# Kernel tuning notes

Hardware: AMD Instinct MI355X
Metric: run time of the kernel (lower is better)

The kernel has to match this reference:

```python
import jax, jax.numpy as jnp
import numpy as np

N_HEADS = 32
N_KV_HEADS = 8
HEAD_DIM = 128
DIM = 4096
ROPE_THETA = 500000.0
B, S = 2, 2048


def setup_inputs() -> dict:
    key = jax.random.key(0)
    k1, k2, k3, k4, k5 = jax.random.split(key, 5)
    sd = 0.02
    return {
        "x": jax.random.normal(k1, (B, S, DIM), dtype=jnp.float32),
        "wq": jax.random.normal(k2, (DIM, N_HEADS * HEAD_DIM), dtype=jnp.float32) * sd,
        "wk": jax.random.normal(k3, (DIM, N_KV_HEADS * HEAD_DIM), dtype=jnp.float32) * sd,
        "wv": jax.random.normal(k4, (DIM, N_KV_HEADS * HEAD_DIM), dtype=jnp.float32) * sd,
        "wo": jax.random.normal(k5, (N_HEADS * HEAD_DIM, DIM), dtype=jnp.float32) * sd,
    }


def _rope_freqs(seqlen, head_dim, theta):
    inv = 1.0 / (theta ** (jnp.arange(0, head_dim, 2, dtype=jnp.float32) / head_dim))
    ang = jnp.arange(seqlen, dtype=jnp.float32)[:, None] * inv[None, :]  # [S, hd/2]
    return jnp.cos(ang), jnp.sin(ang)


def _apply_rope(t, cos, sin):
    # t: [B, S, H, hd]; complex multiply on interleaved (even, odd) pairs
    tr = t.reshape(*t.shape[:-1], HEAD_DIM // 2, 2)
    a, b = tr[..., 0], tr[..., 1]
    c = cos[None, :, None, :]
    s = sin[None, :, None, :]
    out = jnp.stack([a * c - b * s, a * s + b * c], axis=-1)
    return out.reshape(t.shape)


def reference(x, wq, wk, wv, wo):
    bsz, seqlen, _ = x.shape
    n_rep = N_HEADS // N_KV_HEADS
    q = (x @ wq).reshape(bsz, seqlen, N_HEADS, HEAD_DIM)
    k = (x @ wk).reshape(bsz, seqlen, N_KV_HEADS, HEAD_DIM)
    v = (x @ wv).reshape(bsz, seqlen, N_KV_HEADS, HEAD_DIM)

    cos, sin = _rope_freqs(seqlen, HEAD_DIM, ROPE_THETA)
    q = _apply_rope(q, cos, sin)
    k = _apply_rope(k, cos, sin)

    # repeat_kv: expand kv heads to n_heads (torch.repeat_interleave dim=2)
    k = jnp.repeat(k, n_rep, axis=2)  # [B, S, H, hd]
    v = jnp.repeat(v, n_rep, axis=2)

    scale = 1.0 / jnp.sqrt(jnp.float32(HEAD_DIM))
    scores = jnp.einsum("bqhd,bkhd->bhqk", q, k) * scale  # [B, H, S, S]
    causal = jnp.tril(jnp.ones((seqlen, seqlen), dtype=bool))
    scores = jnp.where(causal[None, None], scores, jnp.float32(-1e9))
    probs = jax.nn.softmax(scores, axis=-1)
    out = jnp.einsum("bhqk,bkhd->bqhd", probs, v)  # [B, S, H, hd]
    out = out.reshape(bsz, seqlen, N_HEADS * HEAD_DIM)
    return out @ wo
```

## Files before the change

kernel.cpp:

```cpp
#include <hip/hip_runtime.h>
#include <stdint.h>

typedef unsigned short u16;
using short8 = __attribute__((ext_vector_type(8))) short;
using f32x4  = __attribute__((ext_vector_type(4))) float;

#define S_LEN 2048
#define NH 32
#define NKV 8
#define HD 128
#define DIM 4096
#define NQ 4096
#define NKVD 1024

typedef __attribute__((address_space(1))) unsigned int uGLB;
typedef __attribute__((address_space(3))) unsigned int uLDS;

__device__ __forceinline__ void g2l16(const u16* g, u16* l) {
  __builtin_amdgcn_global_load_lds((const uGLB*)g, (uLDS*)l, 16, 0, 0);
}

__device__ __forceinline__ float b2f(u16 u) {
  union { unsigned u32; float f; } x; x.u32 = ((unsigned)u) << 16; return x.f;
}
__device__ __forceinline__ u16 f2b(float f) {
  union { float f; unsigned u32; } x; x.f = f;
  unsigned lsb = (x.u32 >> 16) & 1u;
  x.u32 += 0x7fffu + lsb;
  return (u16)(x.u32 >> 16);
}

__global__ __launch_bounds__(256) void transpose_cast(const float* __restrict__ in,
                                                      u16* __restrict__ out,
                                                      int K, int N) {
  __shared__ float tile[32][33];
  int n0 = blockIdx.x * 32, k0 = blockIdx.y * 32;
  int tx = threadIdx.x, ty = threadIdx.y;
#pragma unroll
  for (int j = 0; j < 4; ++j)
    tile[ty + j * 8][tx] = in[(size_t)(k0 + ty + j * 8) * N + n0 + tx];
  __syncthreads();
#pragma unroll
  for (int j = 0; j < 4; ++j)
    out[(size_t)(n0 + ty + j * 8) * K + k0 + tx] = f2b(tile[tx][ty + j * 8]);
}

__global__ __launch_bounds__(256) void cast_x(const float* __restrict__ in,
                                              u16* __restrict__ out, int n4) {
  int i = blockIdx.x * 256 + threadIdx.x;
  if (i >= n4) return;
  float4 v = reinterpret_cast<const float4*>(in)[i];
  ushort4 u;
  u.x = f2b(v.x); u.y = f2b(v.y); u.z = f2b(v.z); u.w = f2b(v.w);
  reinterpret_cast<ushort4*>(out)[i] = u;
}

__global__ __launch_bounds__(256, 2) void gemm_bt(const u16* __restrict__ A,
                                                  const u16* __restrict__ Bt,
                                                  int N, int mode,
                                                  float* __restrict__ out,
                                                  u16* __restrict__ Qb,
                                                  u16* __restrict__ Kb,
                                                  u16* __restrict__ Vt) {
  const int K = 4096;
  __shared__ __align__(16) u16 As[128 * 32];
  __shared__ __align__(16) u16 Bs[128 * 32];
  int tid  = threadIdx.x;
  int m0   = blockIdx.y * 128, n0 = blockIdx.x * 128;
  int lane = tid & 63, w = tid >> 6;
  int wr   = w >> 1, wc = w & 1;
  int ml   = lane & 15, quad = lane >> 4;

  f32x4 acc[4][4] = {};

  for (int k0 = 0; k0 < K; k0 += 32) {
    __syncthreads();
#pragma unroll
    for (int p = 0; p < 2; ++p) {
      int slot = w * 128 + p * 64 + lane;
      int row = slot >> 2, ch = slot & 3;
      int src = ch ^ ((row >> 1) & 3);
      g2l16(A + (size_t)(m0 + row) * K + k0 + src * 8, &As[(w * 128 + p * 64) * 8]);
      g2l16(Bt + (size_t)(n0 + row) * K + k0 + src * 8, &Bs[(w * 128 + p * 64) * 8]);
    }
    __syncthreads();
    short8 af[4], bfr[4];
#pragma unroll
    for (int mi = 0; mi < 4; ++mi) {
      int row = wr * 64 + mi * 16 + ml;
      int ch = quad ^ ((row >> 1) & 3);
      af[mi] = *reinterpret_cast<const short8*>(&As[row * 32 + ch * 8]);
    }
#pragma unroll
    for (int ni = 0; ni < 4; ++ni) {
      int row = wc * 64 + ni * 16 + ml;
      int ch = quad ^ ((row >> 1) & 3);
      bfr[ni] = *reinterpret_cast<const short8*>(&Bs[row * 32 + ch * 8]);
    }
#pragma unroll
    for (int mi = 0; mi < 4; ++mi)
#pragma unroll
      for (int ni = 0; ni < 4; ++ni)
        acc[mi][ni] = __builtin_amdgcn_mfma_f32_16x16x32_bf16(af[mi], bfr[ni], acc[mi][ni], 0, 0, 0);
  }

#pragma unroll
  for (int mi = 0; mi < 4; ++mi) {
#pragma unroll
    for (int ni = 0; ni < 4; ++ni) {
#pragma unroll
      for (int r = 0; r < 4; ++r) {
        int row = m0 + wr * 64 + mi * 16 + quad * 4 + r;
        int col = n0 + wc * 64 + ni * 16 + ml;
        float v = acc[mi][ni][r];
        if (mode == 1) {
          out[(size_t)row * N + col] = v;
        } else {
          int b = row >> 11, s = row & (S_LEN - 1);
          if (col < NQ) {
            int h = col >> 7, d = col & 127;
            Qb[((size_t)((b * NH + h) * S_LEN + s)) * HD + d] = f2b(v);
          } else if (col < NQ + NKVD) {
            int cc = col - NQ; int h = cc >> 7, d = cc & 127;
            Kb[((size_t)((b * NKV + h) * S_LEN + s)) * HD + d] = f2b(v);
          } else {
            int cc = col - NQ - NKVD; int h = cc >> 7, d = cc & 127;
            Vt[((size_t)((b * NKV + h) * HD + d)) * S_LEN + s] = f2b(v);
          }
        }
      }
    }
  }
}

__global__ __launch_bounds__(256) void rope_ip(u16* __restrict__ X, int npairs) {
  int idx = blockIdx.x * 256 + threadIdx.x;
  if (idx >= npairs) return;
  int i = idx & 63;
  int s = (idx >> 6) & (S_LEN - 1);
  float inv = __expf(-0.2050369278939421f * (float)i);
  float ang = (float)s * inv;
  float sn, cs;
  sincosf(ang, &sn, &cs);
  ushort2 pr = reinterpret_cast<ushort2*>(X)[idx];
  float a = b2f(pr.x), b = b2f(pr.y);
  ushort2 o;
  o.x = f2b(a * cs - b * sn);
  o.y = f2b(a * sn + b * cs);
  reinterpret_cast<ushort2*>(X)[idx] = o;
}

__global__ __launch_bounds__(256, 3) void flash(const u16* __restrict__ Qb,
                                                const u16* __restrict__ Kb,
                                                const u16* __restrict__ Vt,
                                                u16* __restrict__ AO) {
  __shared__ __align__(16) u16 Ks[64 * 128];
  __shared__ __align__(16) u16 Vs[128 * 64];
  __shared__ __align__(16) u16 Ps[4 * 16 * 80];

  int tid  = threadIdx.x;
  int lane = tid & 63, w = tid >> 6;
  int ml   = lane & 15, quad = lane >> 4;
  int q_tile = blockIdx.x, h = blockIdx.y, b = blockIdx.z;
  int hkv = h >> 2;
  int q0  = q_tile * 64;
  const u16* Qh = Qb + ((size_t)(b * NH + h) * S_LEN) * HD;
  const u16* Kh = Kb + ((size_t)(b * NKV + hkv) * S_LEN) * HD;
  const u16* Vh = Vt + ((size_t)(b * NKV + hkv) * HD) * S_LEN;
  u16* Pw = Ps + w * 16 * 80;

  short8 qf[4];
#pragma unroll
  for (int ks = 0; ks < 4; ++ks)
    qf[ks] = *reinterpret_cast<const short8*>(
        Qh + (size_t)(q0 + w * 16 + ml) * HD + ks * 32 + quad * 8);

  short8 ones8;
  {
    u16 one_b = 0x3f80;
#pragma unroll
    for (int j = 0; j < 8; ++j) ones8[j] = (short)one_b;
  }

  f32x4 o[8] = {};
  f32x4 o9 = {};
  const float SC = 0.12751745f;
  const float BIAS = 18.0f;

  int qg = q0 + w * 16 + ml;
  int ntile = q_tile + 1;
  for (int it = 0; it < ntile; ++it) {
    int kv0 = it * 64;
    __syncthreads();
#pragma unroll
    for (int p = 0; p < 4; ++p) {
      int slot = w * 256 + p * 64 + lane;
      int krow = slot >> 4, kch = slot & 15;
      int ksrc = kch ^ (krow & 15);
      g2l16(Kh + (size_t)(kv0 + krow) * HD + ksrc * 8, &Ks[(w * 256 + p * 64) * 8]);
      int vrow = slot >> 3, vch = slot & 7;
      int vsrc = vch ^ (vrow & 7);
      g2l16(Vh + (size_t)vrow * S_LEN + kv0 + vsrc * 8, &Vs[(w * 256 + p * 64) * 8]);
    }
    __syncthreads();

    f32x4 st[4] = {};
#pragma unroll
    for (int ks = 0; ks < 4; ++ks) {
#pragma unroll
      for (int nt = 0; nt < 4; ++nt) {
        int row = nt * 16 + ml;
        int ch = ((ks << 2) | quad) ^ ml;
        short8 kf = *reinterpret_cast<const short8*>(&Ks[row * 128 + ch * 8]);
        st[nt] = __builtin_amdgcn_mfma_f32_16x16x32_bf16(kf, qf[ks], st[nt], 0, 0, 0);
      }
    }

    bool diag = (it == q_tile);
#pragma unroll
    for (int nt = 0; nt < 4; ++nt) {
      float p0 = exp2f(fmaf(st[nt][0], SC, -BIAS));
      float p1 = exp2f(fmaf(st[nt][1], SC, -BIAS));
      float p2 = exp2f(fmaf(st[nt][2], SC, -BIAS));
      float p3 = exp2f(fmaf(st[nt][3], SC, -BIAS));
      if (diag) {
        int kg = kv0 + nt * 16 + quad * 4;
        if (kg + 0 > qg) p0 = 0.f;
        if (kg + 1 > qg) p1 = 0.f;
        if (kg + 2 > qg) p2 = 0.f;
        if (kg + 3 > qg) p3 = 0.f;
      }
      uint2 pk;
      pk.x = (unsigned)f2b(p0) | ((unsigned)f2b(p1) << 16);
      pk.y = (unsigned)f2b(p2) | ((unsigned)f2b(p3) << 16);
      *reinterpret_cast<uint2*>(&Pw[ml * 80 + nt * 16 + quad * 4]) = pk;
    }

#pragma unroll
    for (int ks2 = 0; ks2 < 2; ++ks2) {
      short8 pf = *reinterpret_cast<const short8*>(&Pw[ml * 80 + ks2 * 32 + quad * 8]);
#pragma unroll
      for (int dt = 0; dt < 8; ++dt) {
        int row = dt * 16 + ml;
        int ch = ((ks2 << 2) | quad) ^ (ml & 7);
        short8 vf = *reinterpret_cast<const short8*>(&Vs[row * 64 + ch * 8]);
        o[dt] = __builtin_amdgcn_mfma_f32_16x16x32_bf16(pf, vf, o[dt], 0, 0, 0);
      }
      o9 = __builtin_amdgcn_mfma_f32_16x16x32_bf16(pf, ones8, o9, 0, 0, 0);
    }
  }

  size_t row_base = (size_t)(b * S_LEN + q0 + w * 16 + quad * 4);
#pragma unroll
  for (int r = 0; r < 4; ++r) {
    float inv_l = 1.0f / o9[r];
#pragma unroll
    for (int dt = 0; dt < 8; ++dt) {
      int col = h * HD + dt * 16 + ml;
      AO[(row_base + r) * (size_t)DIM + col] = f2b(o[dt][r] * inv_l);
    }
  }
}

extern "C" void kernel_launch(void* const* d_in, const int* in_sizes, int n_in,
                              void* d_out, int out_size, void* d_ws, size_t ws_size,
                              hipStream_t stream) {
  const float* x  = (const float*)d_in[0];
  const float* wq = (const float*)d_in[1];
  const float* wk = (const float*)d_in[2];
  const float* wv = (const float*)d_in[3];
  const float* wo = (const float*)d_in[4];
  float* out = (float*)d_out;
  char* ws = (char*)d_ws;

  u16* Wqt = (u16*)(ws + 0);
  u16* Wkt = (u16*)(ws + 33554432);
  u16* Wvt = (u16*)(ws + 41943040);
  u16* Xb  = (u16*)(ws + 50331648);
  u16* Qb  = (u16*)(ws + 83886080);
  u16* Kb  = (u16*)(ws + 117440512);
  u16* Vt  = (u16*)(ws + 125829120);

  transpose_cast<<<dim3(128, 128), dim3(32, 8), 0, stream>>>(wq, Wqt, 4096, 4096);
  transpose_cast<<<dim3(32, 128),  dim3(32, 8), 0, stream>>>(wk, Wkt, 4096, 1024);
  transpose_cast<<<dim3(32, 128),  dim3(32, 8), 0, stream>>>(wv, Wvt, 4096, 1024);
  cast_x<<<16384, 256, 0, stream>>>(x, Xb, 4194304);

  gemm_bt<<<dim3(48, 32), 256, 0, stream>>>(Xb, Wqt, 6144, 0, nullptr, Qb, Kb, Vt);

  rope_ip<<<32768, 256, 0, stream>>>(Qb, 8388608);
  rope_ip<<<8192, 256, 0, stream>>>(Kb, 2097152);

  transpose_cast<<<dim3(128, 128), dim3(32, 8), 0, stream>>>(wo, Wqt, 4096, 4096);

  flash<<<dim3(32, 32, 2), 256, 0, stream>>>(Qb, Kb, Vt, Xb);

  gemm_bt<<<dim3(32, 32), 256, 0, stream>>>(Xb, Wqt, 4096, 1, out, nullptr, nullptr, nullptr);
}
```

Measured before the change: 874.0 us.

## Replace 128x128 GEMM with 256x256 double-buffered pipelined 8-wave kernel

Replaces the 128x128-tile, single-buffered GEMM with a 256x256-tile, 512-thread kernel. It uses a 64-wide K step, double-buffered LDS with staged global_load_lds prefetch interleaved between four MFMA quadrants, s_setprio around the MFMA bursts, and XCD-aware block remapping. The aim is more data reuse per tile and overlap of global loads with MFMA work in both the QKV and output projections. In exchange it uses 64KB of LDS per block and 128 accumulators per thread, and it gives fewer workgroups (384 and 256) relative to the CU count.

```diff
diff --git a/kernel.cpp b/kernel.cpp
--- a/kernel.cpp
+++ b/kernel.cpp
@@ -55,63 +55,149 @@
   reinterpret_cast<ushort4*>(out)[i] = u;
 }
 
-__global__ __launch_bounds__(256, 2) void gemm_bt(const u16* __restrict__ A,
-                                                  const u16* __restrict__ Bt,
-                                                  int N, int mode,
-                                                  float* __restrict__ out,
-                                                  u16* __restrict__ Qb,
-                                                  u16* __restrict__ Kb,
-                                                  u16* __restrict__ Vt) {
+__global__ __launch_bounds__(512) void gemm256(const u16* __restrict__ A,
+                                               const u16* __restrict__ Bt,
+                                               int N, int mode,
+                                               float* __restrict__ out,
+                                               u16* __restrict__ Qb,
+                                               u16* __restrict__ Kb,
+                                               u16* __restrict__ Vt) {
   const int K = 4096;
-  __shared__ __align__(16) u16 As[128 * 32];
-  __shared__ __align__(16) u16 Bs[128 * 32];
+  const int NT = 64;
+  __shared__ __align__(16) u16 lds[2][2][2][8192];
+
   int tid  = threadIdx.x;
-  int m0   = blockIdx.y * 128, n0 = blockIdx.x * 128;
   int lane = tid & 63, w = tid >> 6;
-  int wr   = w >> 1, wc = w & 1;
   int ml   = lane & 15, quad = lane >> 4;
-
-  f32x4 acc[4][4] = {};
-
-  for (int k0 = 0; k0 < K; k0 += 32) {
-    __syncthreads();
-#pragma unroll
-    for (int p = 0; p < 2; ++p) {
-      int slot = w * 128 + p * 64 + lane;
-      int row = slot >> 2, ch = slot & 3;
-      int src = ch ^ ((row >> 1) & 3);
-      g2l16(A + (size_t)(m0 + row) * K + k0 + src * 8, &As[(w * 128 + p * 64) * 8]);
-      g2l16(Bt + (size_t)(n0 + row) * K + k0 + src * 8, &Bs[(w * 128 + p * 64) * 8]);
-    }
-    __syncthreads();
-    short8 af[4], bfr[4];
-#pragma unroll
-    for (int mi = 0; mi < 4; ++mi) {
-      int row = wr * 64 + mi * 16 + ml;
-      int ch = quad ^ ((row >> 1) & 3);
-      af[mi] = *reinterpret_cast<const short8*>(&As[row * 32 + ch * 8]);
-    }
+  int wm   = w >> 2, wn = w & 3;
+
+  int nwg = gridDim.x * gridDim.y;
+  int bid = blockIdx.y * gridDim.x + blockIdx.x;
+  int sbid = (bid & 7) * (nwg >> 3) + (bid >> 3);
+  int bx = sbid % gridDim.x, by = sbid / gridDim.x;
+  int m0 = by * 256, n0 = bx * 256;
+
+  int dst  = w * 1024 + lane * 16;
+  int lg   = dst ^ (((lane >> 5) & 1) << 5);
+  int srow = lg >> 7, scol = (lg & 127) >> 1;
+  const u16* pA = A  + (size_t)(m0 + srow) * K + scol;
+  const u16* pB = Bt + (size_t)(n0 + srow) * K + scol;
+
+#define STAGE(mat, T, hh) do { \
+    int _b = (T) & 1; \
+    int _Tc = (T) < NT ? (T) : (NT - 1); \
+    const u16* _s = ((mat) ? pB : pA) + (size_t)(hh) * 128 * K + (size_t)_Tc * 64; \
+    u16* _d = &lds[_b][mat][hh][w * 512]; \
+    g2l16(_s, _d); \
+    g2l16(_s + (size_t)64 * K, _d + 4096); \
+  } while (0)
+
+  f32x4 acc[8][4] = {};
+  int rxor = ((ml >> 2) & 1) << 5;
+  int aoff = ml * 128 + ((quad * 16) ^ rxor);
+  int boff = (wn & 1) * 8192 + aoff;
+
+  STAGE(0, 0, 0); STAGE(0, 0, 1); STAGE(1, 0, 0); STAGE(1, 0, 1);
+  STAGE(0, 1, 0);
+  asm volatile("s_waitcnt vmcnt(2)" ::: "memory");
+  __builtin_amdgcn_s_barrier();
+
+  short8 af[4][2], bf0[2][2], bf1[2][2];
+
+  for (int t = 0; t < NT; ++t) {
+    int buf = t & 1;
+    const char* Ab = reinterpret_cast<const char*>(&lds[buf][0][wm][0]);
+    const char* Bb = reinterpret_cast<const char*>(&lds[buf][1][wn >> 1][0]);
+
+#pragma unroll
+    for (int mi = 0; mi < 4; ++mi)
+#pragma unroll
+      for (int ks = 0; ks < 2; ++ks)
+        af[mi][ks] = *reinterpret_cast<const short8*>(Ab + aoff + mi * 2048 + ks * 64);
+#pragma unroll
+    for (int ni = 0; ni < 2; ++ni)
+#pragma unroll
+      for (int ks = 0; ks < 2; ++ks)
+        bf0[ni][ks] = *reinterpret_cast<const short8*>(Bb + boff + ni * 2048 + ks * 64);
+    STAGE(0, t + 1, 1);
+    __builtin_amdgcn_s_barrier();
+    asm volatile("s_waitcnt lgkmcnt(0)" ::: "memory");
+    __builtin_amdgcn_sched_barrier(0);
+    __builtin_amdgcn_s_setprio(1);
+#pragma unroll
+    for (int mi = 0; mi < 4; ++mi)
+#pragma unroll
+      for (int ni = 0; ni < 2; ++ni)
+#pragma unroll
+        for (int ks = 0; ks < 2; ++ks)
+          acc[mi][ni] = __builtin_amdgcn_mfma_f32_16x16x32_bf16(af[mi][ks], bf0[ni][ks], acc[mi][ni], 0, 0, 0);
+    __builtin_amdgcn_s_setprio(0);
+    __builtin_amdgcn_s_barrier();
+
+#pragma unroll
+    for (int ni = 0; ni < 2; ++ni)
+#pragma unroll
+      for (int ks = 0; ks < 2; ++ks)
+        bf1[ni][ks] = *reinterpret_cast<const short8*>(Bb + boff + (2 + ni) * 2048 + ks * 64);
+    STAGE(1, t + 1, 0);
+    __builtin_amdgcn_s_barrier();
+    asm volatile("s_waitcnt lgkmcnt(0)" ::: "memory");
+    __builtin_amdgcn_sched_barrier(0);
+    __builtin_amdgcn_s_setprio(1);
+#pragma unroll
+    for (int mi = 0; mi < 4; ++mi)
+#pragma unroll
+      for (int ni = 0; ni < 2; ++ni)
+#pragma unroll
+        for (int ks = 0; ks < 2; ++ks)
+          acc[mi][2 + ni] = __builtin_amdgcn_mfma_f32_16x16x32_bf16(af[mi][ks], bf1[ni][ks], acc[mi][2 + ni], 0, 0, 0);
+    __builtin_amdgcn_s_setprio(0);
+    __builtin_amdgcn_s_barrier();
+
+#pragma unroll
+    for (int mi = 0; mi < 4; ++mi)
+#pragma unroll
+      for (int ks = 0; ks < 2; ++ks)
+        af[mi][ks] = *reinterpret_cast<const short8*>(Ab + aoff + 8192 + mi * 2048 + ks * 64);
+    STAGE(1, t + 1, 1);
+    __builtin_amdgcn_s_barrier();
+    asm volatile("s_waitcnt lgkmcnt(0)" ::: "memory");
+    __builtin_amdgcn_sched_barrier(0);
+    __builtin_amdgcn_s_setprio(1);
+#pragma unroll
+    for (int mi = 0; mi < 4; ++mi)
+#pragma unroll
+      for (int ni = 0; ni < 2; ++ni)
+#pragma unroll
+        for (int ks = 0; ks < 2; ++ks)
+          acc[4 + mi][ni] = __builtin_amdgcn_mfma_f32_16x16x32_bf16(af[mi][ks], bf0[ni][ks], acc[4 + mi][ni], 0, 0, 0);
+    __builtin_amdgcn_s_setprio(0);
+    __builtin_amdgcn_s_barrier();
+
+    STAGE(0, t + 2, 0);
+    __builtin_amdgcn_s_barrier();
+    __builtin_amdgcn_s_setprio(1);
+#pragma unroll
+    for (int mi = 0; mi < 4; ++mi)
+#pragma unroll
+      for (int ni = 0; ni < 2; ++ni)
+#pragma unroll
+        for (int ks = 0; ks < 2; ++ks)
+          acc[4 + mi][2 + ni] = __builtin_amdgcn_mfma_f32_16x16x32_bf16(af[mi][ks], bf1[ni][ks], acc[4 + mi][2 + ni], 0, 0, 0);
+    __builtin_amdgcn_s_setprio(0);
+    asm volatile("s_waitcnt vmcnt(2)" ::: "memory");
+    __builtin_amdgcn_s_barrier();
+  }
+#undef STAGE
+
+#pragma unroll
+  for (int mi = 0; mi < 8; ++mi) {
 #pragma unroll
     for (int ni = 0; ni < 4; ++ni) {
-      int row = wc * 64 + ni * 16 + ml;
-      int ch = quad ^ ((row >> 1) & 3);
-      bfr[ni] = *reinterpret_cast<const short8*>(&Bs[row * 32 + ch * 8]);
-    }
-#pragma unroll
-    for (int mi = 0; mi < 4; ++mi)
-#pragma unroll
-      for (int ni = 0; ni < 4; ++ni)
-        acc[mi][ni] = __builtin_amdgcn_mfma_f32_16x16x32_bf16(af[mi], bfr[ni], acc[mi][ni], 0, 0, 0);
-  }
-
-#pragma unroll
-  for (int mi = 0; mi < 4; ++mi) {
-#pragma unroll
-    for (int ni = 0; ni < 4; ++ni) {
 #pragma unroll
       for (int r = 0; r < 4; ++r) {
-        int row = m0 + wr * 64 + mi * 16 + quad * 4 + r;
-        int col = n0 + wc * 64 + ni * 16 + ml;
+        int row = m0 + wm * 128 + mi * 16 + quad * 4 + r;
+        int col = n0 + wn * 64 + ni * 16 + ml;
         float v = acc[mi][ni][r];
         if (mode == 1) {
           out[(size_t)row * N + col] = v;
@@ -286,7 +372,7 @@
   transpose_cast<<<dim3(32, 128),  dim3(32, 8), 0, stream>>>(wv, Wvt, 4096, 1024);
   cast_x<<<16384, 256, 0, stream>>>(x, Xb, 4194304);
 
-  gemm_bt<<<dim3(48, 32), 256, 0, stream>>>(Xb, Wqt, 6144, 0, nullptr, Qb, Kb, Vt);
+  gemm256<<<dim3(24, 16), 512, 0, stream>>>(Xb, Wqt, 6144, 0, nullptr, Qb, Kb, Vt);
 
   rope_ip<<<32768, 256, 0, stream>>>(Qb, 8388608);
   rope_ip<<<8192, 256, 0, stream>>>(Kb, 2097152);
@@ -295,5 +381,5 @@
 
   flash<<<dim3(32, 32, 2), 256, 0, stream>>>(Qb, Kb, Vt, Xb);
 
-  gemm_bt<<<dim3(32, 32), 256, 0, stream>>>(Xb, Wqt, 4096, 1, out, nullptr, nullptr, nullptr);
-}
+  gemm256<<<dim3(16, 16), 512, 0, stream>>>(Xb, Wqt, 4096, 1, out, nullptr, nullptr, nullptr);
+}
```

Result: faster. 850.6 us (-2.7%).
